# Optimization experiments

Measured on AMD Instinct MI355X. Metric: run time of the kernel, lower is better.

The kernel has to match this reference:

```python
import jax, jax.numpy as jnp
import numpy as np

B, H, IN = 2048, 256, 64
K_TERMS = 8


def setup_inputs() -> dict:
    key = jax.random.key(0)
    ks = jax.random.split(key, 8)
    limit_x = float(np.sqrt(6.0 / (IN + H)))
    limit_h = float(np.sqrt(6.0 / (H + H)))
    return {
        "h": jax.random.normal(ks[0], (B, H), dtype=jnp.float32),
        "x": jax.random.normal(ks[1], (B, IN), dtype=jnp.float32),
        "xdot": jax.random.normal(ks[2], (B, IN), dtype=jnp.float32),
        "wx": jax.random.uniform(ks[3], (H, IN), minval=-limit_x, maxval=limit_x, dtype=jnp.float32),
        "wh": jax.random.uniform(ks[4], (H, H), minval=-limit_h, maxval=limit_h, dtype=jnp.float32),
        "wout": jax.random.uniform(ks[5], (H, H), minval=-limit_h, maxval=limit_h, dtype=jnp.float32),
        "b0": jnp.zeros((H,), dtype=jnp.float32),
        "b1": jnp.zeros((H,), dtype=jnp.float32),
    }


def reference(h, x, xdot, wx, wh, wout, b0, b1):
    # Batched version of the per-sample vector field (original is vmapped by the solver).
    l1 = x @ wx.T + h @ wh.T + b0                 # [B,H]
    relu_val = jax.nn.relu(l1)
    lout = relu_val @ wout.T + b1                 # [B,H]
    tanh_val = jnp.tanh(lout)
    dtanh = 1.0 - tanh_val ** 2                   # [B,H]
    drelu = (l1 > 0).astype(jnp.float32)          # activation == 'relu' (hard gate)
    # d_outer[b,i,j] = dtanh[b,i] * wout[i,j] * drelu[b,j]
    d_outer = dtanh[:, :, None] * wout[None, :, :] * drelu[:, None, :]  # [B,H,H]
    Jx = jnp.einsum('bhj,ji->bhi', d_outer, wx)   # [B,H,IN]
    Jh = jnp.einsum('bhj,ji->bhi', d_outer, wh)   # [B,H,H]
    jx = jnp.einsum('bhi,bi->bh', Jx, xdot)       # [B,H]
    h_dot = jx
    curr_term = jx
    for _ in range(K_TERMS):
        curr_term = jnp.einsum('bij,bj->bi', Jh, curr_term)
        h_dot = h_dot + curr_term
    return h_dot
```

## Files before the change

kernel.cpp:

```cpp
#include <hip/hip_runtime.h>
#include <math.h>

#define B_  2048
#define H_  256
#define IN_ 64

typedef __attribute__((ext_vector_type(8))) short bf8_t;
typedef __attribute__((ext_vector_type(4))) short s4_t;
typedef __attribute__((ext_vector_type(4))) float f4_t;

#define MFMA_BF16(a, b, c) __builtin_amdgcn_mfma_f32_16x16x32_bf16((a), (b), (c), 0, 0, 0)

__device__ __forceinline__ short f2bf(float f) {
  union { float f; unsigned u; } v; v.f = f;
  unsigned u = v.u + 0x7fffu + ((v.u >> 16) & 1u);
  return (short)(u >> 16);
}
__device__ __forceinline__ float bf2f(short s) {
  union { unsigned u; float f; } v; v.u = ((unsigned)(unsigned short)s) << 16;
  return v.f;
}

__device__ __align__(16) short g_whf[2][65536];
__device__ __align__(16) short g_wof[2][65536];
__device__ __align__(16) short g_wxf[2][16384];

__global__ void prep_frag(const float* __restrict__ wh, const float* __restrict__ wo,
                          const float* __restrict__ wx) {
  int tid = blockIdx.x * 256 + threadIdx.x;
  const float* W; short* Dh; short* Dl; int ld, ksh, o8;
  if (tid < 8192)       { W = wh; Dh = g_whf[0]; Dl = g_whf[1]; ld = 256; ksh = 3; o8 = tid; }
  else if (tid < 16384) { W = wo; Dh = g_wof[0]; Dl = g_wof[1]; ld = 256; ksh = 3; o8 = tid - 8192; }
  else if (tid < 18432) { W = wx; Dh = g_wxf[0]; Dl = g_wxf[1]; ld = 64;  ksh = 1; o8 = tid - 16384; }
  else return;
  int lane = o8 & 63;
  int gks = o8 >> 6;
  int g = gks >> ksh, ks = gks & ((1 << ksh) - 1);
  int c = g * 16 + (lane & 15);
  int k0 = ks * 32 + ((lane >> 4) & 3) * 8;
  const float* p = W + (size_t)c * ld + k0;
  bf8_t hi, lo;
#pragma unroll
  for (int j = 0; j < 8; ++j) {
    float f = p[j];
    short h = f2bf(f);
    hi[j] = h; lo[j] = f2bf(f - bf2f(h));
  }
  *reinterpret_cast<bf8_t*>(Dh + (size_t)o8 * 8) = hi;
  *reinterpret_cast<bf8_t*>(Dl + (size_t)o8 * 8) = lo;
}

#define GEMM3(A0, A1, AH, AL, WH, WL, NK) do {                                  \
  f4_t q0 = {0.f,0.f,0.f,0.f}, q1 = {0.f,0.f,0.f,0.f};                          \
  _Pragma("unroll")                                                             \
  for (int ks = 0; ks < (NK); ++ks) {                                           \
    bf8_t ah = *reinterpret_cast<const bf8_t*>(&AH[ln][ks * 32 + lq * 8]);      \
    bf8_t al = *reinterpret_cast<const bf8_t*>(&AL[ln][ks * 32 + lq * 8]);      \
    if (ks & 1) {                                                               \
      q0 = MFMA_BF16(ah, WH[0][ks], q0); q0 = MFMA_BF16(ah, WL[0][ks], q0);     \
      q0 = MFMA_BF16(al, WH[0][ks], q0);                                        \
      q1 = MFMA_BF16(ah, WH[1][ks], q1); q1 = MFMA_BF16(ah, WL[1][ks], q1);     \
      q1 = MFMA_BF16(al, WH[1][ks], q1);                                        \
    } else {                                                                    \
      A0 = MFMA_BF16(ah, WH[0][ks], A0); A0 = MFMA_BF16(ah, WL[0][ks], A0);     \
      A0 = MFMA_BF16(al, WH[0][ks], A0);                                        \
      A1 = MFMA_BF16(ah, WH[1][ks], A1); A1 = MFMA_BF16(ah, WL[1][ks], A1);     \
      A1 = MFMA_BF16(al, WH[1][ks], A1);                                        \
    }                                                                           \
  }                                                                             \
  A0 = A0 + q0; A1 = A1 + q1; } while (0)

#define GEMM2(A0, A1, AH, AL, WH, NK) do {                                      \
  f4_t q0 = {0.f,0.f,0.f,0.f}, q1 = {0.f,0.f,0.f,0.f};                          \
  _Pragma("unroll")                                                             \
  for (int ks = 0; ks < (NK); ++ks) {                                           \
    bf8_t ah = *reinterpret_cast<const bf8_t*>(&AH[ln][ks * 32 + lq * 8]);      \
    bf8_t al = *reinterpret_cast<const bf8_t*>(&AL[ln][ks * 32 + lq * 8]);      \
    if (ks & 1) {                                                               \
      q0 = MFMA_BF16(ah, WH[0][ks], q0); q0 = MFMA_BF16(al, WH[0][ks], q0);     \
      q1 = MFMA_BF16(ah, WH[1][ks], q1); q1 = MFMA_BF16(al, WH[1][ks], q1);     \
    } else {                                                                    \
      A0 = MFMA_BF16(ah, WH[0][ks], A0); A0 = MFMA_BF16(al, WH[0][ks], A0);     \
      A1 = MFMA_BF16(ah, WH[1][ks], A1); A1 = MFMA_BF16(al, WH[1][ks], A1);     \
    }                                                                           \
  }                                                                             \
  A0 = A0 + q0; A1 = A1 + q1; } while (0)

#define GEMM1(A0, A1, AH, WH, NK) do {                                          \
  f4_t q0 = {0.f,0.f,0.f,0.f}, q1 = {0.f,0.f,0.f,0.f};                          \
  _Pragma("unroll")                                                             \
  for (int ks = 0; ks < (NK); ++ks) {                                           \
    bf8_t ah = *reinterpret_cast<const bf8_t*>(&AH[ln][ks * 32 + lq * 8]);      \
    if (ks & 1) {                                                               \
      q0 = MFMA_BF16(ah, WH[0][ks], q0);                                        \
      q1 = MFMA_BF16(ah, WH[1][ks], q1);                                        \
    } else {                                                                    \
      A0 = MFMA_BF16(ah, WH[0][ks], A0);                                        \
      A1 = MFMA_BF16(ah, WH[1][ks], A1);                                        \
    }                                                                           \
  }                                                                             \
  A0 = A0 + q0; A1 = A1 + q1; } while (0)

__global__ __launch_bounds__(512, 2) void jacde_mfma(
    const float* __restrict__ h_g, const float* __restrict__ x_g,
    const float* __restrict__ xd_g, const float* __restrict__ wx,
    const float* __restrict__ wh, const float* __restrict__ b0,
    const float* __restrict__ b1, float* __restrict__ out) {

  __shared__ short h_hi[16][264], h_lo[16][264];
  __shared__ short x_hi[16][72],  x_lo[16][72];
  __shared__ short xd_hi[16][72], xd_lo[16][72];
  __shared__ short u_hi[16][264], u_lo[16][264];
  __shared__ short v_hi[16][264];
  __shared__ float l1_t[16][264];
  __shared__ int   fix_cnt;
  __shared__ int   fix_list[64];

  short (*vb)[264] = reinterpret_cast<short (*)[264]>(l1_t);

  const int tid  = threadIdx.x;
  const int wv   = tid >> 6;
  const int lane = tid & 63;
  const int ln   = lane & 15;
  const int lq   = lane >> 4;
  const int r0   = blockIdx.x * 16;
  const int cbase = wv * 32;

  if (tid == 0) fix_cnt = 0;

  for (int c = tid; c < 16 * 64; c += 512) {
    int r = c >> 6, k4 = (c & 63) * 4;
    f4_t v = *reinterpret_cast<const f4_t*>(h_g + (size_t)(r0 + r) * H_ + k4);
    s4_t shv, slv;
#pragma unroll
    for (int j = 0; j < 4; ++j) { short h = f2bf(v[j]); shv[j] = h; slv[j] = f2bf(v[j] - bf2f(h)); }
    *reinterpret_cast<s4_t*>(&h_hi[r][k4]) = shv;
    *reinterpret_cast<s4_t*>(&h_lo[r][k4]) = slv;
  }
  {
    int t2 = tid & 255;
    const float* src = (tid < 256) ? x_g : xd_g;
    short (*dh)[72] = (tid < 256) ? x_hi : xd_hi;
    short (*dl)[72] = (tid < 256) ? x_lo : xd_lo;
    int r = t2 >> 4, k4 = (t2 & 15) * 4;
    f4_t v = *reinterpret_cast<const f4_t*>(src + (size_t)(r0 + r) * IN_ + k4);
    s4_t shv, slv;
#pragma unroll
    for (int j = 0; j < 4; ++j) { short h = f2bf(v[j]); shv[j] = h; slv[j] = f2bf(v[j] - bf2f(h)); }
    *reinterpret_cast<s4_t*>(&dh[r][k4]) = shv;
    *reinterpret_cast<s4_t*>(&dl[r][k4]) = slv;
  }

  bf8_t whf[2][8], wof[2][8], wol[2][8];
  f4_t acc0, acc1, sacc0, sacc1;
  float dre0[4], dre1[4], dta0[4], dta1[4], hd0[4], hd1[4];

  {
    bf8_t whl[2][8], wxh[2][2], wxl[2][2];
#pragma unroll
    for (int t = 0; t < 2; ++t) {
      int gb = wv * 2 + t;
#pragma unroll
      for (int ks = 0; ks < 8; ++ks) {
        int off = ((gb * 8 + ks) * 64 + lane) * 8;
        whf[t][ks] = *reinterpret_cast<const bf8_t*>(&g_whf[0][off]);
        whl[t][ks] = *reinterpret_cast<const bf8_t*>(&g_whf[1][off]);
      }
#pragma unroll
      for (int ks = 0; ks < 2; ++ks) {
        int off = ((gb * 2 + ks) * 64 + lane) * 8;
        wxh[t][ks] = *reinterpret_cast<const bf8_t*>(&g_wxf[0][off]);
        wxl[t][ks] = *reinterpret_cast<const bf8_t*>(&g_wxf[1][off]);
      }
    }
    __syncthreads();

    float bv0 = b0[cbase + ln], bv1 = b0[cbase + 16 + ln];
    acc0 = (f4_t){bv0, bv0, bv0, bv0};
    acc1 = (f4_t){bv1, bv1, bv1, bv1};
    GEMM3(acc0, acc1, h_hi, h_lo, whf, whl, 8);
    GEMM3(acc0, acc1, x_hi, x_lo, wxh, wxl, 2);
    sacc0 = (f4_t){0.f, 0.f, 0.f, 0.f};
    sacc1 = (f4_t){0.f, 0.f, 0.f, 0.f};
    GEMM3(sacc0, sacc1, xd_hi, xd_lo, wxh, wxl, 2);
#pragma unroll
    for (int r = 0; r < 4; ++r) {
      l1_t[lq * 4 + r][cbase + ln]      = acc0[r];
      l1_t[lq * 4 + r][cbase + 16 + ln] = acc1[r];
      if (fabsf(acc0[r]) < 1e-4f) {
        int idx = atomicAdd(&fix_cnt, 1);
        if (idx < 64) fix_list[idx] = ((lq * 4 + r) << 8) | (cbase + ln);
      }
      if (fabsf(acc1[r]) < 1e-4f) {
        int idx = atomicAdd(&fix_cnt, 1);
        if (idx < 64) fix_list[idx] = ((lq * 4 + r) << 8) | (cbase + 16 + ln);
      }
    }
  }

#pragma unroll
  for (int t = 0; t < 2; ++t) {
    int gb = wv * 2 + t;
#pragma unroll
    for (int ks = 0; ks < 8; ++ks) {
      int off = ((gb * 8 + ks) * 64 + lane) * 8;
      wof[t][ks] = *reinterpret_cast<const bf8_t*>(&g_wof[0][off]);
      wol[t][ks] = *reinterpret_cast<const bf8_t*>(&g_wof[1][off]);
    }
  }
  __syncthreads();

  {
    int nfix = min(fix_cnt, 64);
    for (int e = wv; e < nfix; e += 8) {
      int rc = fix_list[e];
      int r = rc >> 8, c = rc & 255;
      const float* hrow = h_g + (size_t)(r0 + r) * H_;
      const float* wrow = wh + (size_t)c * H_;
      double sum = (double)hrow[lane]       * (double)wrow[lane]
                 + (double)hrow[lane + 64]  * (double)wrow[lane + 64]
                 + (double)hrow[lane + 128] * (double)wrow[lane + 128]
                 + (double)hrow[lane + 192] * (double)wrow[lane + 192]
                 + (double)x_g[(size_t)(r0 + r) * IN_ + lane] * (double)wx[(size_t)c * IN_ + lane];
#pragma unroll
      for (int m = 32; m; m >>= 1) sum += __shfl_xor(sum, m);
      if (lane == 0) l1_t[r][c] = (float)(sum + (double)b0[c]);
    }
  }
  __syncthreads();

#pragma unroll
  for (int r = 0; r < 4; ++r) {
    int row = lq * 4 + r;
    float l10 = l1_t[row][cbase + ln];
    float l11 = l1_t[row][cbase + 16 + ln];
    dre0[r] = (l10 > 0.f) ? 1.f : 0.f;
    dre1[r] = (l11 > 0.f) ? 1.f : 0.f;
    float rv0 = l10 > 0.f ? l10 : 0.f;
    float rv1 = l11 > 0.f ? l11 : 0.f;
    short rh0 = f2bf(rv0), rh1 = f2bf(rv1);
    u_hi[row][cbase + ln]      = rh0;  u_lo[row][cbase + ln]      = f2bf(rv0 - bf2f(rh0));
    u_hi[row][cbase + 16 + ln] = rh1;  u_lo[row][cbase + 16 + ln] = f2bf(rv1 - bf2f(rh1));
    float u00 = dre0[r] * sacc0[r];
    float u01 = dre1[r] * sacc1[r];
    short uh0 = f2bf(u00), uh1 = f2bf(u01);
    h_hi[row][cbase + ln]      = uh0;  h_lo[row][cbase + ln]      = f2bf(u00 - bf2f(uh0));
    h_hi[row][cbase + 16 + ln] = uh1;  h_lo[row][cbase + 16 + ln] = f2bf(u01 - bf2f(uh1));
  }
  __syncthreads();

  {
    float bv0 = b1[cbase + ln], bv1 = b1[cbase + 16 + ln];
    acc0 = (f4_t){bv0, bv0, bv0, bv0};
    acc1 = (f4_t){bv1, bv1, bv1, bv1};
    GEMM3(acc0, acc1, u_hi, u_lo, wof, wol, 8);
    sacc0 = (f4_t){0.f, 0.f, 0.f, 0.f};
    sacc1 = (f4_t){0.f, 0.f, 0.f, 0.f};
    GEMM2(sacc0, sacc1, h_hi, h_lo, wof, 8);
#pragma unroll
    for (int r = 0; r < 4; ++r) {
      float t0 = tanhf(acc0[r]);
      float t1 = tanhf(acc1[r]);
      dta0[r] = 1.f - t0 * t0;
      dta1[r] = 1.f - t1 * t1;
      int row = lq * 4 + r;
      float v0 = dta0[r] * sacc0[r];
      float v1 = dta1[r] * sacc1[r];
      hd0[r] = v0; hd1[r] = v1;
      vb[row][cbase + ln]      = f2bf(v0);
      vb[row][cbase + 16 + ln] = f2bf(v1);
    }
  }
  __syncthreads();

  const short (*vsrc)[264] = vb;
  for (int it = 0; it < 8; ++it) {
    acc0 = (f4_t){0.f, 0.f, 0.f, 0.f};
    acc1 = (f4_t){0.f, 0.f, 0.f, 0.f};
    GEMM1(acc0, acc1, vsrc, whf, 8);
#pragma unroll
    for (int r = 0; r < 4; ++r) {
      int row = lq * 4 + r;
      u_hi[row][cbase + ln]      = f2bf(dre0[r] * acc0[r]);
      u_hi[row][cbase + 16 + ln] = f2bf(dre1[r] * acc1[r]);
    }
    __syncthreads();

    acc0 = (f4_t){0.f, 0.f, 0.f, 0.f};
    acc1 = (f4_t){0.f, 0.f, 0.f, 0.f};
    GEMM1(acc0, acc1, u_hi, wof, 8);
#pragma unroll
    for (int r = 0; r < 4; ++r) {
      int row = lq * 4 + r;
      float v0 = dta0[r] * acc0[r];
      float v1 = dta1[r] * acc1[r];
      hd0[r] += v0; hd1[r] += v1;
      if (it < 7) {
        v_hi[row][cbase + ln]      = f2bf(v0);
        v_hi[row][cbase + 16 + ln] = f2bf(v1);
      }
    }
    vsrc = v_hi;
    __syncthreads();
  }

#pragma unroll
  for (int r = 0; r < 4; ++r) {
    int row = lq * 4 + r;
    out[(size_t)(r0 + row) * H_ + cbase + ln]      = hd0[r];
    out[(size_t)(r0 + row) * H_ + cbase + 16 + ln] = hd1[r];
  }
}

extern "C" void kernel_launch(void* const* d_in, const int* in_sizes, int n_in,
                              void* d_out, int out_size, void* d_ws, size_t ws_size,
                              hipStream_t stream) {
  const float* h_g  = (const float*)d_in[0];
  const float* x_g  = (const float*)d_in[1];
  const float* xd_g = (const float*)d_in[2];
  const float* wx   = (const float*)d_in[3];
  const float* wh   = (const float*)d_in[4];
  const float* wo   = (const float*)d_in[5];
  const float* b0   = (const float*)d_in[6];
  const float* b1   = (const float*)d_in[7];
  prep_frag<<<dim3(72), dim3(256), 0, stream>>>(wh, wo, wx);
  jacde_mfma<<<dim3(B_ / 16), dim3(512), 0, stream>>>(
      h_g, x_g, xd_g, wx, wh, b0, b1, (float*)d_out);
}
```

Before: 89.35 us.

## Process four batch rows per block to quadruple grid size

Each block now handles 4 batch rows instead of 16. The grid grows to 512 blocks, which should occupy more CUs on the 256-CU device. Rows 4-15 of the MFMA tiles are zero-padded in shared memory, and only the lq==0 lanes do fix-up detection and output writes. In exchange, three quarters of the MFMA work is wasted on padding, and each block still loads the full weight fragments, so weight traffic per row rises fourfold. The b1 bias load is also hoisted earlier.

```diff
diff --git a/kernel.cpp b/kernel.cpp
--- a/kernel.cpp
+++ b/kernel.cpp
@@ -123,26 +123,26 @@
   const int lane = tid & 63;
   const int ln   = lane & 15;
   const int lq   = lane >> 4;
-  const int r0   = blockIdx.x * 16;
+  const int r0   = blockIdx.x * 4;
   const int cbase = wv * 32;
 
   if (tid == 0) fix_cnt = 0;
 
-  for (int c = tid; c < 16 * 64; c += 512) {
-    int r = c >> 6, k4 = (c & 63) * 4;
+  if (tid < 256) {
+    int r = tid >> 6, k4 = (tid & 63) * 4;
     f4_t v = *reinterpret_cast<const f4_t*>(h_g + (size_t)(r0 + r) * H_ + k4);
     s4_t shv, slv;
 #pragma unroll
     for (int j = 0; j < 4; ++j) { short h = f2bf(v[j]); shv[j] = h; slv[j] = f2bf(v[j] - bf2f(h)); }
     *reinterpret_cast<s4_t*>(&h_hi[r][k4]) = shv;
     *reinterpret_cast<s4_t*>(&h_lo[r][k4]) = slv;
-  }
-  {
-    int t2 = tid & 255;
-    const float* src = (tid < 256) ? x_g : xd_g;
-    short (*dh)[72] = (tid < 256) ? x_hi : xd_hi;
-    short (*dl)[72] = (tid < 256) ? x_lo : xd_lo;
-    int r = t2 >> 4, k4 = (t2 & 15) * 4;
+  } else if (tid < 384) {
+    int t2 = tid - 256;
+    const float* src = (t2 < 64) ? x_g : xd_g;
+    short (*dh)[72] = (t2 < 64) ? x_hi : xd_hi;
+    short (*dl)[72] = (t2 < 64) ? x_lo : xd_lo;
+    int t3 = t2 & 63;
+    int r = t3 >> 4, k4 = (t3 & 15) * 4;
     f4_t v = *reinterpret_cast<const f4_t*>(src + (size_t)(r0 + r) * IN_ + k4);
     s4_t shv, slv;
 #pragma unroll
@@ -150,10 +150,28 @@
     *reinterpret_cast<s4_t*>(&dh[r][k4]) = shv;
     *reinterpret_cast<s4_t*>(&dl[r][k4]) = slv;
   }
+  {
+    const s4_t z4 = {0, 0, 0, 0};
+    for (int e = tid; e < 2448; e += 512) {
+      if (e < 1584) {
+        int i = e; short (*D)[264] = h_hi;
+        if (i >= 792) { i -= 792; D = h_lo; }
+        *reinterpret_cast<s4_t*>(&D[4 + i / 66][(i % 66) * 4]) = z4;
+      } else {
+        int i = e - 1584;
+        short (*D)[72] = x_hi;
+        if (i >= 648)      { i -= 648; D = xd_lo; }
+        else if (i >= 432) { i -= 432; D = xd_hi; }
+        else if (i >= 216) { i -= 216; D = x_lo; }
+        *reinterpret_cast<s4_t*>(&D[4 + i / 18][(i % 18) * 4]) = z4;
+      }
+    }
+  }
 
   bf8_t whf[2][8], wof[2][8], wol[2][8];
   f4_t acc0, acc1, sacc0, sacc1;
   float dre0[4], dre1[4], dta0[4], dta1[4], hd0[4], hd1[4];
+  float bv1a, bv1b;
 
   {
     bf8_t whl[2][8], wxh[2][2], wxl[2][2];
@@ -187,17 +205,21 @@
     for (int r = 0; r < 4; ++r) {
       l1_t[lq * 4 + r][cbase + ln]      = acc0[r];
       l1_t[lq * 4 + r][cbase + 16 + ln] = acc1[r];
-      if (fabsf(acc0[r]) < 1e-4f) {
-        int idx = atomicAdd(&fix_cnt, 1);
-        if (idx < 64) fix_list[idx] = ((lq * 4 + r) << 8) | (cbase + ln);
-      }
-      if (fabsf(acc1[r]) < 1e-4f) {
-        int idx = atomicAdd(&fix_cnt, 1);
-        if (idx < 64) fix_list[idx] = ((lq * 4 + r) << 8) | (cbase + 16 + ln);
-      }
-    }
-  }
-
+      if (lq == 0) {
+        if (fabsf(acc0[r]) < 1e-4f) {
+          int idx = atomicAdd(&fix_cnt, 1);
+          if (idx < 64) fix_list[idx] = (r << 8) | (cbase + ln);
+        }
+        if (fabsf(acc1[r]) < 1e-4f) {
+          int idx = atomicAdd(&fix_cnt, 1);
+          if (idx < 64) fix_list[idx] = (r << 8) | (cbase + 16 + ln);
+        }
+      }
+    }
+  }
+
+  bv1a = b1[cbase + ln];
+  bv1b = b1[cbase + 16 + ln];
 #pragma unroll
   for (int t = 0; t < 2; ++t) {
     int gb = wv * 2 + t;
@@ -250,9 +272,8 @@
   __syncthreads();
 
   {
-    float bv0 = b1[cbase + ln], bv1 = b1[cbase + 16 + ln];
-    acc0 = (f4_t){bv0, bv0, bv0, bv0};
-    acc1 = (f4_t){bv1, bv1, bv1, bv1};
+    acc0 = (f4_t){bv1a, bv1a, bv1a, bv1a};
+    acc1 = (f4_t){bv1b, bv1b, bv1b, bv1b};
     GEMM3(acc0, acc1, u_hi, u_lo, wof, wol, 8);
     sacc0 = (f4_t){0.f, 0.f, 0.f, 0.f};
     sacc1 = (f4_t){0.f, 0.f, 0.f, 0.f};
@@ -304,11 +325,12 @@
     __syncthreads();
   }
 
-#pragma unroll
-  for (int r = 0; r < 4; ++r) {
-    int row = lq * 4 + r;
-    out[(size_t)(r0 + row) * H_ + cbase + ln]      = hd0[r];
-    out[(size_t)(r0 + row) * H_ + cbase + 16 + ln] = hd1[r];
+  if (lq == 0) {
+#pragma unroll
+    for (int r = 0; r < 4; ++r) {
+      out[(size_t)(r0 + r) * H_ + cbase + ln]      = hd0[r];
+      out[(size_t)(r0 + r) * H_ + cbase + 16 + ln] = hd1[r];
+    }
   }
 }
 
@@ -324,6 +346,6 @@
   const float* b0   = (const float*)d_in[6];
   const float* b1   = (const float*)d_in[7];
   prep_frag<<<dim3(72), dim3(256), 0, stream>>>(wh, wo, wx);
-  jacde_mfma<<<dim3(B_ / 16), dim3(512), 0, stream>>>(
+  jacde_mfma<<<dim3(B_ / 4), dim3(512), 0, stream>>>(
       h_g, x_g, xd_g, wx, wh, b0, b1, (float*)d_out);
 }
```

After: 108.0 us. 1.21x slower.
